# Performance work log

Measured on AMD Instinct MI355X. Metric: run time of the kernel, lower is better.

## Reference

```python
import jax, jax.numpy as jnp
import numpy as np

SHIFT = 8  # shift_range init kwarg
EPS = 1e-12  # F.normalize default eps (x / max(||x||, eps))


def setup_inputs() -> dict:
    key = jax.random.key(0)
    k1, k2 = jax.random.split(key)
    grd_feature = jax.random.normal(k1, (64, 64, 24, 24), dtype=jnp.float32)
    sat_feature = jax.random.normal(k2, (64, 64, 64, 64), dtype=jnp.float32)
    return {"grd_feature": grd_feature, "sat_feature": sat_feature}


def reference(grd_feature, sat_feature):
    M, C, Hs, Ws = sat_feature.shape
    N, _, H, W = grd_feature.shape
    kH = min(H, Hs - 2 * SHIFT, 24)
    kW = min(W, Ws - 2 * SHIFT, 24)
    # center-crop ground features to kernel size
    grd = grd_feature[:, :, H // 2 - kH // 2: H // 2 + kH // 2,
                      W // 2 - kW // 2: W // 2 + kW // 2]  # [N,C,kH,kW]
    # crop sat features to search window (kernel + 2*shift)
    sat = sat_feature[:, :, Hs // 2 - SHIFT - kH // 2: Hs // 2 + SHIFT + kH // 2,
                      Ws // 2 - SHIFT - kW // 2: Ws // 2 + SHIFT + kW // 2]  # [M,C,Hi,Wi]
    # cross-correlation: repeat+grouped-conv in torch == plain conv2d here -> [M,N,Ho,Wo]
    corr = jax.lax.conv_general_dilated(
        sat, grd, window_strides=(1, 1), padding='VALID',
        dimension_numbers=('NCHW', 'OIHW', 'NCHW'))
    Ho, Wo = corr.shape[2], corr.shape[3]
    flat_idx = jnp.argmax(corr.reshape(M, N, Ho * Wo), axis=-1)  # [M,N]
    hy = flat_idx // Wo
    wx = flat_idx % Wo

    def gather_patch(sat_j, h, w):  # sat_j: [C,Hi,Wi]
        return jax.lax.dynamic_slice(sat_j, (0, h, w), (C, kH, kW))

    # vectorized patch gather over (M, N) -> [M,N,C,kH,kW]
    patches = jax.vmap(
        lambda sj, hs, ws: jax.vmap(lambda h, w: gather_patch(sj, h, w))(hs, ws)
    )(sat, hy, wx)

    pn = patches.reshape(M * N, -1)
    pn = pn / jnp.maximum(jnp.linalg.norm(pn, axis=-1, keepdims=True), EPS)
    pn = pn.reshape(M, N, C, kH, kW)
    gn = grd.reshape(N, -1)
    gn = gn / jnp.maximum(jnp.linalg.norm(gn, axis=-1, keepdims=True), EPS)
    gn = gn.reshape(N, C, kH, kW)
    similarity_matrix = jnp.einsum('mnchw,nchw->mn', pn, gn)
    sat_f = patches[M - 1, N - 1]  # last gathered (unnormalized) patch, as in torch
    return similarity_matrix, sat_f
```

## Files before the change

kernel.cpp:

```cpp
#include <hip/hip_runtime.h>
#include <hip/hip_bf16.h>
#include <math.h>


typedef float f32x16 __attribute__((ext_vector_type(16)));
typedef short short8 __attribute__((ext_vector_type(8)));

#define SATT_H 0u
#define GRDT_H 3276800u
#define CORR_O 4456448u
#define WIN2_O 5701632u
#define GN2_O  5720128u
#define IDX_O  5720192u
#define CEX_O  5721216u

__global__ __launch_bounds__(256) void make_satT(const float* __restrict__ sat,
                                                 __hip_bfloat16* __restrict__ sth) {
    __shared__ __hip_bfloat16 th[40 * 66];
    int m = blockIdx.x / 40, r = blockIdx.x % 40;
    int tid = threadIdx.x;
    const float* base = sat + (size_t)m * 262144 + (12 + r) * 64 + 12;
    for (int k = 0; k < 10; k++) {
        int idx = tid + 256 * k;
        int c = idx / 40, w2 = idx % 40;
        th[w2 * 66 + c] = __float2bfloat16(base[c * 4096 + w2]);
    }
    __syncthreads();
    __hip_bfloat16* dh = sth + (size_t)m * 102400 + r * 640;
    for (int k = 0; k < 10; k++) {
        int idx = tid + 256 * k;
        int cc = idx / 640, rem = idx - cc * 640;
        int w2 = rem >> 4, cl = rem & 15;
        dh[cc * 25600 + w2 * 16 + cl] = th[w2 * 66 + cc * 16 + cl];
    }
}

__global__ __launch_bounds__(256) void make_grdT(const float* __restrict__ grd,
                                                 __hip_bfloat16* __restrict__ gth,
                                                 float* __restrict__ gn2) {
    __shared__ __hip_bfloat16 t[32 * 577];
    __shared__ float red[4];
    int bid = blockIdx.x;
    int n = bid >> 1, ch = bid & 1;
    int tid = threadIdx.x;
    const float* src = grd + (size_t)n * 36864 + ch * 32 * 576;
    float s = 0.0f;
    for (int k = 0; k < 72; k++) {
        int idx = tid + 256 * k;
        int cl = idx / 576, ij = idx % 576;
        float v = src[idx];
        s += v * v;
        t[cl * 577 + ij] = __float2bfloat16(v);
    }
    for (int off = 32; off; off >>= 1) s += __shfl_down(s, off);
    if ((tid & 63) == 0) red[tid >> 6] = s;
    __syncthreads();
    if (tid == 0) atomicAdd(&gn2[n], red[0] + red[1] + red[2] + red[3]);
    for (int k = 0; k < 72; k++) {
        int idx = tid + 256 * k;
        int ij = idx >> 5, cl = idx & 31;
        int c = ch * 32 + cl;
        gth[((size_t)((c >> 4) * 576 + ij)) * 1024 + n * 16 + (c & 15)] = t[cl * 577 + ij];
    }
}

__global__ __launch_bounds__(256) void make_win2(const __hip_bfloat16* __restrict__ sth,
                                                 float* __restrict__ win2) {
    __shared__ float S2[40][41];
    __shared__ float RS[40][18];
    int m = blockIdx.x, tid = threadIdx.x;
    const __hip_bfloat16* base = sth + (size_t)m * 102400;
    for (int k = 0; k < 7; k++) {
        int pix = tid + 256 * k;
        if (pix < 1600) {
            float s = 0.0f;
            for (int cc = 0; cc < 4; cc++) {
                const __hip_bfloat16* p = base + cc * 25600 + pix * 16;
                for (int cl = 0; cl < 16; cl++) {
                    float v = __bfloat162float(p[cl]);
                    s += v * v;
                }
            }
            S2[pix / 40][pix % 40] = s;
        }
    }
    __syncthreads();
    for (int k = 0; k < 3; k++) {
        int idx = tid + 256 * k;
        if (idx < 680) {
            int r = idx / 17, x = idx % 17;
            float s = 0.0f;
            for (int j = 0; j < 24; j++) s += S2[r][x + j];
            RS[r][x] = s;
        }
    }
    __syncthreads();
    for (int k = 0; k < 2; k++) {
        int idx = tid + 256 * k;
        if (idx < 289) {
            int y = idx / 17, x = idx % 17;
            float s = 0.0f;
            for (int i2 = 0; i2 < 24; i2++) s += RS[y + i2][x];
            win2[m * 289 + idx] = s;
        }
    }
}

__global__ __launch_bounds__(256, 2) void corr_mfma(const __hip_bfloat16* __restrict__ sth,
                                                    const __hip_bfloat16* __restrict__ gth,
                                                    float* __restrict__ corr) {
    __shared__ __align__(16) __hip_bfloat16 satW[760 * 16];

    int bid = blockIdx.x;
    int xcd = bid & 7, slot = bid >> 3;
    int m = xcd * 8 + (slot >> 3), iq = slot & 7;
    int tid = threadIdx.x;
    int w = tid >> 6, l = tid & 63;
    int ln31 = l & 31, h = l >> 5;

    int rowbase[3];
#pragma unroll
    for (int t = 0; t < 3; t++) {
        int p = (w + 4 * t) * 32 + ln31;
        if (p > 288) p = 288;
        rowbase[t] = (p / 17) * 40 + (p % 17);
    }
    f32x16 acc[3][2];
#pragma unroll
    for (int t = 0; t < 3; t++) {
        acc[t][0] = (f32x16)0.0f;
        acc[t][1] = (f32x16)0.0f;
    }

    const __hip_bfloat16* gbase = gth + (size_t)(iq * 72) * 1024 + ln31 * 16 + h * 8;

#define BLOADR(B0, B1, CC, IJL) {                                               \
        const __hip_bfloat16* p_ = gbase + ((size_t)(CC) * 576 + (IJL)) * 1024; \
        B0 = *(const short8*)p_;                                                \
        B1 = *(const short8*)(p_ + 512);                                        \
    }
#define COMPUTE(IJL, B0, B1) {                                                  \
        int il_ = (IJL) / 24;                                                   \
        int pixoff_ = il_ * 40 + ((IJL) - il_ * 24);                            \
        if (w < 2) {                                                            \
            _Pragma("unroll")                                                   \
            for (int t = 0; t < 3; t++) {                                       \
                int ao = (rowbase[t] + pixoff_) * 32 + h * 16;                  \
                short8 af = *(const short8*)((const char*)satW + ao);           \
                acc[t][0] = __builtin_amdgcn_mfma_f32_32x32x16_bf16(af, B0, acc[t][0], 0, 0, 0); \
                acc[t][1] = __builtin_amdgcn_mfma_f32_32x32x16_bf16(af, B1, acc[t][1], 0, 0, 0); \
            }                                                                   \
        } else {                                                                \
            _Pragma("unroll")                                                   \
            for (int t = 0; t < 2; t++) {                                       \
                int ao = (rowbase[t] + pixoff_) * 32 + h * 16;                  \
                short8 af = *(const short8*)((const char*)satW + ao);           \
                acc[t][0] = __builtin_amdgcn_mfma_f32_32x32x16_bf16(af, B0, acc[t][0], 0, 0, 0); \
                acc[t][1] = __builtin_amdgcn_mfma_f32_32x32x16_bf16(af, B1, acc[t][1], 0, 0, 0); \
            }                                                                   \
        }                                                                       \
    }

#pragma unroll
    for (int cc = 0; cc < 4; cc++) {
        __syncthreads();
        const __hip_bfloat16* satb = sth + (size_t)m * 102400 + cc * 25600 + iq * 1920;
#pragma unroll
        for (int k2 = 0; k2 < 6; k2++) {
            int s = tid + 256 * k2;
            if (s < 1520) {
                float4 v = *(const float4*)(satb + s * 8);
                *(float4*)((char*)satW + s * 16) = v;
            }
        }
        short8 x0, x1, y0, y1, z0, z1;
        BLOADR(x0, x1, cc, 0);
        BLOADR(y0, y1, cc, 1);
        BLOADR(z0, z1, cc, 2);
        __syncthreads();

        for (int ijg = 0; ijg < 24; ijg++) {
            int base = ijg * 3;
            COMPUTE(base + 0, x0, x1);
            if (base + 3 < 72) BLOADR(x0, x1, cc, base + 3);
            COMPUTE(base + 1, y0, y1);
            if (base + 4 < 72) BLOADR(y0, y1, cc, base + 4);
            COMPUTE(base + 2, z0, z1);
            if (base + 5 < 72) BLOADR(z0, z1, cc, base + 5);
        }
    }

    int T = (w < 2) ? 3 : 2;
#pragma unroll
    for (int t = 0; t < 3; t++) {
        if (t >= T) break;
        int tile = w + 4 * t;
#pragma unroll
        for (int nt = 0; nt < 2; nt++)
#pragma unroll
            for (int q = 0; q < 16; q++) {
                int prow = tile * 32 + (q & 3) + 8 * (q >> 2) + 4 * h;
                if (prow < 289)
                    atomicAdd(&corr[((size_t)m * 304 + prow) * 64 + nt * 32 + ln31],
                              acc[t][nt][q]);
            }
    }
#undef BLOADR
#undef COMPUTE
}

__global__ __launch_bounds__(64) void argsim(const float* __restrict__ corr,
                                             const float* __restrict__ win2,
                                             const float* __restrict__ gn2,
                                             float* __restrict__ out,
                                             int* __restrict__ idxb) {
    int b = blockIdx.x, m = b >> 6, n = b & 63, lane = threadIdx.x;
    float bv = -3.0e38f;
    int bi = 1 << 30;
    for (int k = 0; k < 5; k++) {
        int p = lane + 64 * k;
        if (p < 289) {
            float v = corr[((size_t)m * 304 + p) * 64 + n];
            if (v > bv) { bv = v; bi = p; }
        }
    }
    for (int off = 32; off; off >>= 1) {
        float ov = __shfl_down(bv, off);
        int oi = __shfl_down(bi, off);
        if (ov > bv || (ov == bv && oi < bi)) { bv = ov; bi = oi; }
    }
    if (lane == 0) {
        float np = sqrtf(win2[m * 289 + bi]);
        float ng = sqrtf(gn2[n]);
        out[b] = bv / (fmaxf(np, 1e-12f) * fmaxf(ng, 1e-12f));
        idxb[b] = bi;
    }
}

__global__ __launch_bounds__(256) void exact63(const float* __restrict__ sat,
                                               const float* __restrict__ grd,
                                               float* __restrict__ correx) {
    int p = blockIdx.x;
    int hy = p / 17, wx = p % 17;
    int tid = threadIdx.x;
    const float* satm = sat + (size_t)63 * 262144;
    const float* grdn = grd + (size_t)63 * 36864;
    float dot = 0.0f;
    for (int e = tid; e < 36864; e += 256) {
        int c = e / 576, rem = e - c * 576;
        int i = rem / 24, j = rem - i * 24;
        dot += satm[c * 4096 + (12 + hy + i) * 64 + 12 + wx + j] * grdn[e];
    }
    for (int off = 32; off; off >>= 1) dot += __shfl_down(dot, off);
    __shared__ float red[4];
    if ((tid & 63) == 0) red[tid >> 6] = dot;
    __syncthreads();
    if (tid == 0) correx[p] = red[0] + red[1] + red[2] + red[3];
}

__global__ __launch_bounds__(64) void fix63(const float* __restrict__ correx,
                                            const float* __restrict__ win2,
                                            const float* __restrict__ gn2,
                                            float* __restrict__ out,
                                            int* __restrict__ idxb) {
    int lane = threadIdx.x;
    float bv = -3.0e38f;
    int bi = 1 << 30;
    for (int k = 0; k < 5; k++) {
        int p = lane + 64 * k;
        if (p < 289) {
            float v = correx[p];
            if (v > bv) { bv = v; bi = p; }
        }
    }
    for (int off = 32; off; off >>= 1) {
        float ov = __shfl_down(bv, off);
        int oi = __shfl_down(bi, off);
        if (ov > bv || (ov == bv && oi < bi)) { bv = ov; bi = oi; }
    }
    if (lane == 0) {
        out[4095] = bv / (fmaxf(sqrtf(win2[63 * 289 + bi]), 1e-12f) *
                          fmaxf(sqrtf(gn2[63]), 1e-12f));
        idxb[4095] = bi;
    }
}

__global__ __launch_bounds__(256) void copy_patch(const float* __restrict__ sat,
                                                  const int* __restrict__ idxb,
                                                  float* __restrict__ out) {
    int fidx = idxb[4095];
    int hy = fidx / 17, wx = fidx % 17;
    int e = blockIdx.x * 256 + threadIdx.x;
    int c = e / 576;
    int rem = e - c * 576;
    int rr = rem / 24, col = rem - rr * 24;
    out[4096 + e] = sat[(size_t)(63 * 64 + c) * 4096 + (12 + hy + rr) * 64 + 12 + wx + col];
}

extern "C" void kernel_launch(void* const* d_in, const int* in_sizes, int n_in,
                              void* d_out, int out_size, void* d_ws, size_t ws_size,
                              hipStream_t stream) {
    const float* grd = (const float*)d_in[0];
    const float* sat = (const float*)d_in[1];
    float* out = (float*)d_out;

    float* wsf = (float*)d_ws;
    __hip_bfloat16* sth = (__hip_bfloat16*)(wsf + SATT_H);
    __hip_bfloat16* gth = (__hip_bfloat16*)(wsf + GRDT_H);
    float* corr = wsf + CORR_O;
    float* win2 = wsf + WIN2_O;
    float* gn2  = wsf + GN2_O;
    int*   idxb = (int*)(wsf + IDX_O);
    float* cex  = wsf + CEX_O;

    hipMemsetAsync(corr, 0, (size_t)1263744 * sizeof(float), stream);
    make_satT<<<2560, 256, 0, stream>>>(sat, sth);
    make_grdT<<<128, 256, 0, stream>>>(grd, gth, gn2);
    make_win2<<<64, 256, 0, stream>>>(sth, win2);
    corr_mfma<<<512, 256, 0, stream>>>(sth, gth, corr);
    argsim<<<4096, 64, 0, stream>>>(corr, win2, gn2, out, idxb);
    exact63<<<289, 256, 0, stream>>>(sat, grd, cex);
    fix63<<<1, 64, 0, stream>>>(cex, win2, gn2, out, idxb);
    copy_patch<<<144, 256, 0, stream>>>(sat, idxb, out);
}
```

Measured before the change: 192.2 us.

## Rebalance corr MFMA tiles over six waves, fuse win2 partials and fix63

Reorganizes corr_mfma from 4 waves with uneven 3/2 tile assignment to 6 waves with 2/1 assignment to balance MFMA work and raise occupancy. Per-pixel channel sums of squares are now computed in make_satT from shared memory, so make_win2 no longer re-reads the bf16 transpose. The fix63 argmax is merged into copy_patch, with each block recomputing the argmax to remove one launch. Register pressure under the new launch bounds is a risk.

```diff
diff --git a/kernel.cpp b/kernel.cpp
--- a/kernel.cpp
+++ b/kernel.cpp
@@ -13,9 +13,11 @@
 #define GN2_O  5720128u
 #define IDX_O  5720192u
 #define CEX_O  5721216u
+#define S2G_O  5721600u
 
 __global__ __launch_bounds__(256) void make_satT(const float* __restrict__ sat,
-                                                 __hip_bfloat16* __restrict__ sth) {
+                                                 __hip_bfloat16* __restrict__ sth,
+                                                 float* __restrict__ S2g) {
     __shared__ __hip_bfloat16 th[40 * 66];
     int m = blockIdx.x / 40, r = blockIdx.x % 40;
     int tid = threadIdx.x;
@@ -32,6 +34,14 @@
         int cc = idx / 640, rem = idx - cc * 640;
         int w2 = rem >> 4, cl = rem & 15;
         dh[cc * 25600 + w2 * 16 + cl] = th[w2 * 66 + cc * 16 + cl];
+    }
+    if (tid < 40) {
+        float s = 0.0f;
+        for (int c = 0; c < 64; c++) {
+            float v = __bfloat162float(th[tid * 66 + c]);
+            s += v * v;
+        }
+        S2g[m * 1600 + r * 40 + tid] = s;
     }
 }
 
@@ -64,25 +74,14 @@
     }
 }
 
-__global__ __launch_bounds__(256) void make_win2(const __hip_bfloat16* __restrict__ sth,
+__global__ __launch_bounds__(256) void make_win2(const float* __restrict__ S2g,
                                                  float* __restrict__ win2) {
     __shared__ float S2[40][41];
     __shared__ float RS[40][18];
     int m = blockIdx.x, tid = threadIdx.x;
-    const __hip_bfloat16* base = sth + (size_t)m * 102400;
     for (int k = 0; k < 7; k++) {
-        int pix = tid + 256 * k;
-        if (pix < 1600) {
-            float s = 0.0f;
-            for (int cc = 0; cc < 4; cc++) {
-                const __hip_bfloat16* p = base + cc * 25600 + pix * 16;
-                for (int cl = 0; cl < 16; cl++) {
-                    float v = __bfloat162float(p[cl]);
-                    s += v * v;
-                }
-            }
-            S2[pix / 40][pix % 40] = s;
-        }
+        int idx = tid + 256 * k;
+        if (idx < 1600) S2[idx / 40][idx % 40] = S2g[m * 1600 + idx];
     }
     __syncthreads();
     for (int k = 0; k < 3; k++) {
@@ -106,7 +105,7 @@
     }
 }
 
-__global__ __launch_bounds__(256, 2) void corr_mfma(const __hip_bfloat16* __restrict__ sth,
+__global__ __launch_bounds__(384, 3) void corr_mfma(const __hip_bfloat16* __restrict__ sth,
                                                     const __hip_bfloat16* __restrict__ gth,
                                                     float* __restrict__ corr) {
     __shared__ __align__(16) __hip_bfloat16 satW[760 * 16];
@@ -118,16 +117,17 @@
     int w = tid >> 6, l = tid & 63;
     int ln31 = l & 31, h = l >> 5;
 
-    int rowbase[3];
-#pragma unroll
-    for (int t = 0; t < 3; t++) {
-        int p = (w + 4 * t) * 32 + ln31;
+    int rowbase[2];
+#pragma unroll
+    for (int t = 0; t < 2; t++) {
+        int tile = (w < 4) ? (w + 4 * t) : (w + 4);
+        int p = tile * 32 + ln31;
         if (p > 288) p = 288;
         rowbase[t] = (p / 17) * 40 + (p % 17);
     }
-    f32x16 acc[3][2];
-#pragma unroll
-    for (int t = 0; t < 3; t++) {
+    f32x16 acc[2][2];
+#pragma unroll
+    for (int t = 0; t < 2; t++) {
         acc[t][0] = (f32x16)0.0f;
         acc[t][1] = (f32x16)0.0f;
     }
@@ -142,15 +142,7 @@
 #define COMPUTE(IJL, B0, B1) {                                                  \
         int il_ = (IJL) / 24;                                                   \
         int pixoff_ = il_ * 40 + ((IJL) - il_ * 24);                            \
-        if (w < 2) {                                                            \
-            _Pragma("unroll")                                                   \
-            for (int t = 0; t < 3; t++) {                                       \
-                int ao = (rowbase[t] + pixoff_) * 32 + h * 16;                  \
-                short8 af = *(const short8*)((const char*)satW + ao);           \
-                acc[t][0] = __builtin_amdgcn_mfma_f32_32x32x16_bf16(af, B0, acc[t][0], 0, 0, 0); \
-                acc[t][1] = __builtin_amdgcn_mfma_f32_32x32x16_bf16(af, B1, acc[t][1], 0, 0, 0); \
-            }                                                                   \
-        } else {                                                                \
+        if (w < 4) {                                                            \
             _Pragma("unroll")                                                   \
             for (int t = 0; t < 2; t++) {                                       \
                 int ao = (rowbase[t] + pixoff_) * 32 + h * 16;                  \
@@ -158,6 +150,11 @@
                 acc[t][0] = __builtin_amdgcn_mfma_f32_32x32x16_bf16(af, B0, acc[t][0], 0, 0, 0); \
                 acc[t][1] = __builtin_amdgcn_mfma_f32_32x32x16_bf16(af, B1, acc[t][1], 0, 0, 0); \
             }                                                                   \
+        } else {                                                                \
+            int ao = (rowbase[0] + pixoff_) * 32 + h * 16;                      \
+            short8 af = *(const short8*)((const char*)satW + ao);               \
+            acc[0][0] = __builtin_amdgcn_mfma_f32_32x32x16_bf16(af, B0, acc[0][0], 0, 0, 0); \
+            acc[0][1] = __builtin_amdgcn_mfma_f32_32x32x16_bf16(af, B1, acc[0][1], 0, 0, 0); \
         }                                                                       \
     }
 
@@ -166,8 +163,8 @@
         __syncthreads();
         const __hip_bfloat16* satb = sth + (size_t)m * 102400 + cc * 25600 + iq * 1920;
 #pragma unroll
-        for (int k2 = 0; k2 < 6; k2++) {
-            int s = tid + 256 * k2;
+        for (int k2 = 0; k2 < 4; k2++) {
+            int s = tid + 384 * k2;
             if (s < 1520) {
                 float4 v = *(const float4*)(satb + s * 8);
                 *(float4*)((char*)satW + s * 16) = v;
@@ -190,11 +187,11 @@
         }
     }
 
-    int T = (w < 2) ? 3 : 2;
-#pragma unroll
-    for (int t = 0; t < 3; t++) {
+    int T = (w < 4) ? 2 : 1;
+#pragma unroll
+    for (int t = 0; t < 2; t++) {
         if (t >= T) break;
-        int tile = w + 4 * t;
+        int tile = (w < 4) ? (w + 4 * t) : (w + 4);
 #pragma unroll
         for (int nt = 0; nt < 2; nt++)
 #pragma unroll
@@ -258,39 +255,40 @@
     if (tid == 0) correx[p] = red[0] + red[1] + red[2] + red[3];
 }
 
-__global__ __launch_bounds__(64) void fix63(const float* __restrict__ correx,
-                                            const float* __restrict__ win2,
-                                            const float* __restrict__ gn2,
-                                            float* __restrict__ out,
-                                            int* __restrict__ idxb) {
-    int lane = threadIdx.x;
+__global__ __launch_bounds__(256) void copy_patch(const float* __restrict__ sat,
+                                                  const float* __restrict__ cex,
+                                                  const float* __restrict__ win2,
+                                                  const float* __restrict__ gn2,
+                                                  float* __restrict__ out) {
+    __shared__ float rbv[4];
+    __shared__ int rbi[4];
+    int tid = threadIdx.x;
     float bv = -3.0e38f;
     int bi = 1 << 30;
-    for (int k = 0; k < 5; k++) {
-        int p = lane + 64 * k;
-        if (p < 289) {
-            float v = correx[p];
-            if (v > bv) { bv = v; bi = p; }
-        }
+    for (int p = tid; p < 289; p += 256) {
+        float v = cex[p];
+        if (v > bv) { bv = v; bi = p; }
     }
     for (int off = 32; off; off >>= 1) {
         float ov = __shfl_down(bv, off);
         int oi = __shfl_down(bi, off);
         if (ov > bv || (ov == bv && oi < bi)) { bv = ov; bi = oi; }
     }
-    if (lane == 0) {
-        out[4095] = bv / (fmaxf(sqrtf(win2[63 * 289 + bi]), 1e-12f) *
-                          fmaxf(sqrtf(gn2[63]), 1e-12f));
-        idxb[4095] = bi;
-    }
-}
-
-__global__ __launch_bounds__(256) void copy_patch(const float* __restrict__ sat,
-                                                  const int* __restrict__ idxb,
-                                                  float* __restrict__ out) {
-    int fidx = idxb[4095];
+    if ((tid & 63) == 0) { rbv[tid >> 6] = bv; rbi[tid >> 6] = bi; }
+    __syncthreads();
+    if (tid == 0) {
+        for (int q = 1; q < 4; q++)
+            if (rbv[q] > rbv[0] || (rbv[q] == rbv[0] && rbi[q] < rbi[0])) {
+                rbv[0] = rbv[q]; rbi[0] = rbi[q];
+            }
+        if (blockIdx.x == 0)
+            out[4095] = rbv[0] / (fmaxf(sqrtf(win2[63 * 289 + rbi[0]]), 1e-12f) *
+                                  fmaxf(sqrtf(gn2[63]), 1e-12f));
+    }
+    __syncthreads();
+    int fidx = rbi[0];
     int hy = fidx / 17, wx = fidx % 17;
-    int e = blockIdx.x * 256 + threadIdx.x;
+    int e = blockIdx.x * 256 + tid;
     int c = e / 576;
     int rem = e - c * 576;
     int rr = rem / 24, col = rem - rr * 24;
@@ -312,14 +310,14 @@
     float* gn2  = wsf + GN2_O;
     int*   idxb = (int*)(wsf + IDX_O);
     float* cex  = wsf + CEX_O;
+    float* S2g  = wsf + S2G_O;
 
     hipMemsetAsync(corr, 0, (size_t)1263744 * sizeof(float), stream);
-    make_satT<<<2560, 256, 0, stream>>>(sat, sth);
+    make_satT<<<2560, 256, 0, stream>>>(sat, sth, S2g);
     make_grdT<<<128, 256, 0, stream>>>(grd, gth, gn2);
-    make_win2<<<64, 256, 0, stream>>>(sth, win2);
-    corr_mfma<<<512, 256, 0, stream>>>(sth, gth, corr);
+    make_win2<<<64, 256, 0, stream>>>(S2g, win2);
+    corr_mfma<<<512, 384, 0, stream>>>(sth, gth, corr);
     argsim<<<4096, 64, 0, stream>>>(corr, win2, gn2, out, idxb);
     exact63<<<289, 256, 0, stream>>>(sat, grd, cex);
-    fix63<<<1, 64, 0, stream>>>(cex, win2, gn2, out, idxb);
-    copy_patch<<<144, 256, 0, stream>>>(sat, idxb, out);
-}
+    copy_patch<<<144, 256, 0, stream>>>(sat, cex, win2, gn2, out);
+}
```

Measured after the change: 198.2 us. +3.1%, slower.
